# Kernel tuning notes

Hardware: AMD Instinct MI355X
Metric: run time of the kernel (lower is better)

Reference implementation:

```python
import jax, jax.numpy as jnp
import numpy as np

B, N, E = 128, 196, 2048   # batch, num_features (14x14), encoder_dim
D, A = 512, 512            # decoder_dim, attention_dim


def setup_inputs() -> dict:
    key = jax.random.key(0)
    ks = jax.random.split(key, 8)
    s_e = 1.0 / np.sqrt(E)
    s_d = 1.0 / np.sqrt(D)
    s_a = 1.0 / np.sqrt(A)
    return {
        "encoder_out": jax.random.normal(ks[0], (B, N, E), dtype=jnp.float32),
        "decoder_hidden": jax.random.normal(ks[1], (B, D), dtype=jnp.float32),
        "We": jax.random.uniform(ks[2], (E, A), jnp.float32, -s_e, s_e),
        "be": jax.random.uniform(ks[3], (A,), jnp.float32, -s_e, s_e),
        "Wd": jax.random.uniform(ks[4], (D, A), jnp.float32, -s_d, s_d),
        "bd": jax.random.uniform(ks[5], (A,), jnp.float32, -s_d, s_d),
        "Wf": jax.random.uniform(ks[6], (A, 1), jnp.float32, -s_a, s_a),
        "bf": jax.random.uniform(ks[7], (1,), jnp.float32, -s_a, s_a),
    }


def reference(encoder_out, decoder_hidden, We, be, Wd, bd, Wf, bf):
    # att1: [B,N,A] projection of encoder features
    att1 = jnp.einsum('bne,ea->bna', encoder_out, We) + be
    # att2: [B,A] projection of decoder state, broadcast over N
    att2 = decoder_hidden @ Wd + bd
    att = jnp.tanh(att1 + att2[:, None, :])          # [B,N,A]
    scores = jnp.einsum('bna,ao->bno', att, Wf) + bf  # [B,N,1]
    alpha = jax.nn.softmax(scores, axis=1)            # softmax over num_features
    context = jnp.sum(encoder_out * alpha, axis=1)    # [B,E]
    return (context, alpha)
```

## Files before the change

### kernel.cpp

```cpp
#include <hip/hip_runtime.h>
#include <hip/hip_bf16.h>
#include <stdint.h>

#define B_   128
#define N_   196
#define E_   2048
#define D_   512
#define A_   512
#define MTOT (B_ * N_)

typedef short  short8  __attribute__((ext_vector_type(8)));
typedef float  floatx4 __attribute__((ext_vector_type(4)));

__device__ __forceinline__ unsigned short f2bf(float f) {
    union { float f; uint32_t u; } v; v.f = f;
    uint32_t r = v.u + 0x7FFFu + ((v.u >> 16) & 1u);
    return (unsigned short)(r >> 16);
}

__device__ __forceinline__ uint32_t pkbf(float a, float b) {
    uint32_t ua = __float_as_uint(a) + 0x8000u;
    uint32_t ub = __float_as_uint(b) + 0x8000u;
    return __builtin_amdgcn_perm(ub, ua, 0x07060302u);
}

__global__ void transcvt_k(const float* __restrict__ We, unsigned short* __restrict__ WeT) {
    __shared__ float tile[32][33];
    const int e0 = blockIdx.x * 32, a0 = blockIdx.y * 32;
    const int t = threadIdx.x, tc = t & 31, tr = t >> 5;
#pragma unroll
    for (int i = 0; i < 4; ++i) {
        int r = tr + i * 8;
        tile[r][tc] = We[(size_t)(e0 + r) * A_ + a0 + tc];
    }
    __syncthreads();
#pragma unroll
    for (int i = 0; i < 4; ++i) {
        int r = tr + i * 8;
        WeT[(size_t)(a0 + r) * E_ + e0 + tc] = f2bf(tile[tc][r]);
    }
}

__launch_bounds__(512)
__global__ void att2_k(const float* __restrict__ dh, const float* __restrict__ Wd,
                       const float* __restrict__ bd, const float* __restrict__ be,
                       float* __restrict__ att2p) {
    const int b = blockIdx.x, t = threadIdx.x;
    __shared__ float sdh[D_];
    sdh[t] = dh[b * D_ + t];
    __syncthreads();
    float acc = 0.f;
#pragma unroll 8
    for (int d = 0; d < D_; ++d) acc += sdh[d] * Wd[(size_t)d * A_ + t];
    att2p[(size_t)b * A_ + t] = acc + bd[t] + be[t];
}

__launch_bounds__(512, 4)
__global__ void score_gemm(const float* __restrict__ enc,
                           const unsigned short* __restrict__ WeT,
                           const float* __restrict__ att2p,
                           const float* __restrict__ Wf,
                           float* __restrict__ scoresP) {
    __shared__ __align__(16) char sMem[8192 + 32768];
    __shared__ float sPart[8][64];

    const int t   = threadIdx.x;
    const int w   = t >> 6;
    const int l   = t & 63;
    const int l15 = l & 15;
    const int q4  = l >> 4;
    const int row0 = blockIdx.x * 64;

    floatx4 acc[4][4] = {};

    const float* aSrc;
    int aDst;
    {
        int s = w * 64 + l;
        int r = s >> 3, p = s & 7;
        aSrc = enc + (size_t)(row0 + r) * E_ + ((p ^ (r & 7)) * 4);
        aDst = w * 1024;
    }
    const unsigned short* bSrc[4];
    int bDst[4];
#pragma unroll
    for (int j = 0; j < 4; ++j) {
        int s = (w * 4 + j) * 64 + l;
        int n = s >> 2, p = s & 3;
        int q = p ^ ((n >> 1) & 3);
        bSrc[j] = WeT + (size_t)n * E_ + q * 8;
        bDst[j] = 8192 + (w * 4 + j) * 1024;
    }

    const int pLo   = (2 * q4) ^ (l15 & 7);
    const int offAlo = l15 * 128 + pLo * 16;
    const int offAhi = l15 * 128 + (pLo ^ 1) * 16;
    const int offB   = 8192 + (w * 64 + l15) * 64 + (q4 ^ ((l15 >> 1) & 3)) * 16;

    for (int kk = 0; kk < 64; ++kk) {
        __builtin_amdgcn_global_load_lds(
            (const __attribute__((address_space(1))) uint32_t*)(aSrc + kk * 32),
            (__attribute__((address_space(3))) uint32_t*)(sMem + aDst), 16, 0, 0);
#pragma unroll
        for (int j = 0; j < 4; ++j)
            __builtin_amdgcn_global_load_lds(
                (const __attribute__((address_space(1))) uint32_t*)(bSrc[j] + kk * 32),
                (__attribute__((address_space(3))) uint32_t*)(sMem + bDst[j]), 16, 0, 0);
        __syncthreads();

        short8 bfr[4];
        union { uint32_t u[4]; short8 s; } af[4];
#pragma unroll
        for (int ni = 0; ni < 4; ++ni)
            bfr[ni] = *(const short8*)(sMem + offB + ni * 1024);
#pragma unroll
        for (int mi = 0; mi < 4; ++mi) {
            float4 lo = *(const float4*)(sMem + offAlo + mi * 2048);
            float4 hi = *(const float4*)(sMem + offAhi + mi * 2048);
            af[mi].u[0] = pkbf(lo.x, lo.y);
            af[mi].u[1] = pkbf(lo.z, lo.w);
            af[mi].u[2] = pkbf(hi.x, hi.y);
            af[mi].u[3] = pkbf(hi.z, hi.w);
        }
#pragma unroll
        for (int mi = 0; mi < 4; ++mi) {
            acc[mi][0] = __builtin_amdgcn_mfma_f32_16x16x32_bf16(af[mi].s, bfr[0], acc[mi][0], 0, 0, 0);
            acc[mi][1] = __builtin_amdgcn_mfma_f32_16x16x32_bf16(af[mi].s, bfr[1], acc[mi][1], 0, 0, 0);
            acc[mi][2] = __builtin_amdgcn_mfma_f32_16x16x32_bf16(af[mi].s, bfr[2], acc[mi][2], 0, 0, 0);
            acc[mi][3] = __builtin_amdgcn_mfma_f32_16x16x32_bf16(af[mi].s, bfr[3], acc[mi][3], 0, 0, 0);
        }
        __syncthreads();
    }

    const int cbase = w * 64;
    float wfv[4];
#pragma unroll
    for (int ni = 0; ni < 4; ++ni) wfv[ni] = Wf[cbase + ni * 16 + l15];

#pragma unroll
    for (int mi = 0; mi < 4; ++mi) {
#pragma unroll
        for (int r = 0; r < 4; ++r) {
            const int m    = mi * 16 + q4 * 4 + r;
            const int grow = row0 + m;
            const int bb   = grow / N_;
            const float* a2 = att2p + (size_t)bb * A_ + cbase;
            float s = 0.f;
#pragma unroll
            for (int ni = 0; ni < 4; ++ni) {
                float v  = acc[mi][ni][r] + a2[ni * 16 + l15];
                float e  = __expf(2.f * v);
                float th = 1.f - 2.f / (e + 1.f);
                s += th * wfv[ni];
            }
            s += __shfl_xor(s, 1);
            s += __shfl_xor(s, 2);
            s += __shfl_xor(s, 4);
            s += __shfl_xor(s, 8);
            if (l15 == 0) sPart[w][m] = s;
        }
    }
    __syncthreads();
    if (t < 64) {
        float v = 0.f;
#pragma unroll
        for (int ww = 0; ww < 8; ++ww) v += sPart[ww][t];
        scoresP[row0 + t] = v;
    }
}

__global__ void softmax_k(const float* __restrict__ sp, float* __restrict__ alpha) {
    const int b = blockIdx.x, t = threadIdx.x;
    const int w = t >> 6, l = t & 63;
    __shared__ float red[8];
    float v = -3.0e38f;
    if (t < N_) v = sp[b * N_ + t];
    float m = v;
#pragma unroll
    for (int off = 32; off >= 1; off >>= 1) m = fmaxf(m, __shfl_xor(m, off));
    if (l == 0) red[w] = m;
    __syncthreads();
    m = fmaxf(fmaxf(red[0], red[1]), fmaxf(red[2], red[3]));
    float e = 0.f;
    if (t < N_) e = __expf(v - m);
    float s = e;
#pragma unroll
    for (int off = 32; off >= 1; off >>= 1) s += __shfl_xor(s, off);
    if (l == 0) red[4 + w] = s;
    __syncthreads();
    s = red[4] + red[5] + red[6] + red[7];
    if (t < N_) alpha[b * N_ + t] = e / s;
}

__launch_bounds__(256)
__global__ void context_k(const float* __restrict__ enc, const float* __restrict__ alpha,
                          float* __restrict__ ctx) {
    const int chunk = blockIdx.x, b = blockIdx.y;
    const int t = threadIdx.x, tn = t >> 6, tc = t & 63;
    __shared__ float  sAl[N_];
    __shared__ float4 sRed[256];
    if (t < N_) sAl[t] = alpha[b * N_ + t];
    __syncthreads();
    const float* base = enc + (size_t)b * N_ * E_ + chunk * 256 + tc * 4;
    float4 a = make_float4(0.f, 0.f, 0.f, 0.f);
#pragma unroll 7
    for (int n = tn; n < N_; n += 4) {
        float  al = sAl[n];
        float4 v  = *(const float4*)(base + (size_t)n * E_);
        a.x += al * v.x; a.y += al * v.y; a.z += al * v.z; a.w += al * v.w;
    }
    sRed[t] = a;
    __syncthreads();
    if (t < 64) {
        float4 r0 = sRed[t], r1 = sRed[t + 64], r2 = sRed[t + 128], r3 = sRed[t + 192];
        float4 o = make_float4(r0.x + r1.x + r2.x + r3.x, r0.y + r1.y + r2.y + r3.y,
                               r0.z + r1.z + r2.z + r3.z, r0.w + r1.w + r2.w + r3.w);
        *(float4*)(ctx + (size_t)b * E_ + chunk * 256 + t * 4) = o;
    }
}

extern "C" void kernel_launch(void* const* d_in, const int* in_sizes, int n_in,
                              void* d_out, int out_size, void* d_ws, size_t ws_size,
                              hipStream_t stream) {
    const float* enc = (const float*)d_in[0];
    const float* dh  = (const float*)d_in[1];
    const float* We  = (const float*)d_in[2];
    const float* be  = (const float*)d_in[3];
    const float* Wd  = (const float*)d_in[4];
    const float* bd  = (const float*)d_in[5];
    const float* Wf  = (const float*)d_in[6];

    float* out   = (float*)d_out;
    float* ctx   = out;
    float* alpha = out + B_ * E_;

    char* ws = (char*)d_ws;
    unsigned short* WeT  = (unsigned short*)ws;
    float* att2p         = (float*)(ws + (2u << 20));
    float* scoresP       = (float*)(ws + (2u << 20) + (256u << 10));

    transcvt_k <<<dim3(E_ / 32, A_ / 32), 256, 0, stream>>>(We, WeT);
    att2_k     <<<dim3(B_),              512, 0, stream>>>(dh, Wd, bd, be, att2p);
    score_gemm <<<dim3(MTOT / 64),       512, 0, stream>>>(enc, WeT, att2p, Wf, scoresP);
    softmax_k  <<<dim3(B_),              256, 0, stream>>>(scoresP, alpha);
    context_k  <<<dim3(E_ / 256, B_),    256, 0, stream>>>(enc, alpha, ctx);
}
```

Measured before the change: 440.0 us.

## Register-prefetch pipeline with bf16 double-buffered A tile and direct B loads

```diff
diff --git a/kernel.cpp b/kernel.cpp
--- a/kernel.cpp
+++ b/kernel.cpp
@@ -61,7 +61,7 @@
                            const float* __restrict__ att2p,
                            const float* __restrict__ Wf,
                            float* __restrict__ scoresP) {
-    __shared__ __align__(16) char sMem[8192 + 32768];
+    __shared__ __align__(16) unsigned short sA[2][64 * 32];
     __shared__ float sPart[8][64];
 
     const int t   = threadIdx.x;
@@ -73,66 +73,57 @@
 
     floatx4 acc[4][4] = {};
 
-    const float* aSrc;
-    int aDst;
+    const int ar = t >> 3, ac = t & 7;
+    const float* aG = enc + (size_t)(row0 + ar) * E_ + ac * 4;
+    unsigned short* aW[2] = { &sA[0][ar * 32 + ac * 4], &sA[1][ar * 32 + ac * 4] };
+    const int aRoff = l15 * 32 + q4 * 8;
+
+    const int cbase = w * 64;
+    const unsigned short* pb[4];
+#pragma unroll
+    for (int ni = 0; ni < 4; ++ni)
+        pb[ni] = WeT + (size_t)(cbase + ni * 16 + l15) * E_ + q4 * 8;
+
+    float4 Araw = *(const float4*)(aG);
+    short8 Bcur[4];
+#pragma unroll
+    for (int ni = 0; ni < 4; ++ni) Bcur[ni] = *(const short8*)(pb[ni]);
     {
-        int s = w * 64 + l;
-        int r = s >> 3, p = s & 7;
-        aSrc = enc + (size_t)(row0 + r) * E_ + ((p ^ (r & 7)) * 4);
-        aDst = w * 1024;
-    }
-    const unsigned short* bSrc[4];
-    int bDst[4];
-#pragma unroll
-    for (int j = 0; j < 4; ++j) {
-        int s = (w * 4 + j) * 64 + l;
-        int n = s >> 2, p = s & 3;
-        int q = p ^ ((n >> 1) & 3);
-        bSrc[j] = WeT + (size_t)n * E_ + q * 8;
-        bDst[j] = 8192 + (w * 4 + j) * 1024;
-    }
-
-    const int pLo   = (2 * q4) ^ (l15 & 7);
-    const int offAlo = l15 * 128 + pLo * 16;
-    const int offAhi = l15 * 128 + (pLo ^ 1) * 16;
-    const int offB   = 8192 + (w * 64 + l15) * 64 + (q4 ^ ((l15 >> 1) & 3)) * 16;
+        uint2 hv; hv.x = pkbf(Araw.x, Araw.y); hv.y = pkbf(Araw.z, Araw.w);
+        *(uint2*)aW[0] = hv;
+    }
+    Araw = *(const float4*)(aG + 32);
+    __syncthreads();
 
     for (int kk = 0; kk < 64; ++kk) {
-        __builtin_amdgcn_global_load_lds(
-            (const __attribute__((address_space(1))) uint32_t*)(aSrc + kk * 32),
-            (__attribute__((address_space(3))) uint32_t*)(sMem + aDst), 16, 0, 0);
-#pragma unroll
-        for (int j = 0; j < 4; ++j)
-            __builtin_amdgcn_global_load_lds(
-                (const __attribute__((address_space(1))) uint32_t*)(bSrc[j] + kk * 32),
-                (__attribute__((address_space(3))) uint32_t*)(sMem + bDst[j]), 16, 0, 0);
+        const unsigned short* aBuf = sA[kk & 1];
+        short8 af[4];
+#pragma unroll
+        for (int mi = 0; mi < 4; ++mi)
+            af[mi] = *(const short8*)(aBuf + aRoff + mi * 512);
+        if (kk < 63) {
+            uint2 hv; hv.x = pkbf(Araw.x, Araw.y); hv.y = pkbf(Araw.z, Araw.w);
+            *(uint2*)aW[(kk + 1) & 1] = hv;
+        }
+        if (kk < 62) Araw = *(const float4*)(aG + (kk + 2) * 32);
+        short8 Bn[4];
+        if (kk < 63) {
+#pragma unroll
+            for (int ni = 0; ni < 4; ++ni)
+                Bn[ni] = *(const short8*)(pb[ni] + (kk + 1) * 32);
+        }
+#pragma unroll
+        for (int mi = 0; mi < 4; ++mi) {
+            acc[mi][0] = __builtin_amdgcn_mfma_f32_16x16x32_bf16(af[mi], Bcur[0], acc[mi][0], 0, 0, 0);
+            acc[mi][1] = __builtin_amdgcn_mfma_f32_16x16x32_bf16(af[mi], Bcur[1], acc[mi][1], 0, 0, 0);
+            acc[mi][2] = __builtin_amdgcn_mfma_f32_16x16x32_bf16(af[mi], Bcur[2], acc[mi][2], 0, 0, 0);
+            acc[mi][3] = __builtin_amdgcn_mfma_f32_16x16x32_bf16(af[mi], Bcur[3], acc[mi][3], 0, 0, 0);
+        }
+#pragma unroll
+        for (int ni = 0; ni < 4; ++ni) Bcur[ni] = Bn[ni];
         __syncthreads();
-
-        short8 bfr[4];
-        union { uint32_t u[4]; short8 s; } af[4];
-#pragma unroll
-        for (int ni = 0; ni < 4; ++ni)
-            bfr[ni] = *(const short8*)(sMem + offB + ni * 1024);
-#pragma unroll
-        for (int mi = 0; mi < 4; ++mi) {
-            float4 lo = *(const float4*)(sMem + offAlo + mi * 2048);
-            float4 hi = *(const float4*)(sMem + offAhi + mi * 2048);
-            af[mi].u[0] = pkbf(lo.x, lo.y);
-            af[mi].u[1] = pkbf(lo.z, lo.w);
-            af[mi].u[2] = pkbf(hi.x, hi.y);
-            af[mi].u[3] = pkbf(hi.z, hi.w);
-        }
-#pragma unroll
-        for (int mi = 0; mi < 4; ++mi) {
-            acc[mi][0] = __builtin_amdgcn_mfma_f32_16x16x32_bf16(af[mi].s, bfr[0], acc[mi][0], 0, 0, 0);
-            acc[mi][1] = __builtin_amdgcn_mfma_f32_16x16x32_bf16(af[mi].s, bfr[1], acc[mi][1], 0, 0, 0);
-            acc[mi][2] = __builtin_amdgcn_mfma_f32_16x16x32_bf16(af[mi].s, bfr[2], acc[mi][2], 0, 0, 0);
-            acc[mi][3] = __builtin_amdgcn_mfma_f32_16x16x32_bf16(af[mi].s, bfr[3], acc[mi][3], 0, 0, 0);
-        }
-        __syncthreads();
-    }
-
-    const int cbase = w * 64;
+    }
+
     float wfv[4];
 #pragma unroll
     for (int ni = 0; ni < 4; ++ni) wfv[ni] = Wf[cbase + ni * 16 + l15];
```

Result: slower. 480.2 us (+9.1%).

## Split score GEMM across two column halves with pre-tiled bf16 weight layout

Applied to the files above, without the earlier changes.

```diff
diff --git a/kernel.cpp b/kernel.cpp
--- a/kernel.cpp
+++ b/kernel.cpp
@@ -24,21 +24,20 @@
     return __builtin_amdgcn_perm(ub, ua, 0x07060302u);
 }
 
-__global__ void transcvt_k(const float* __restrict__ We, unsigned short* __restrict__ WeT) {
-    __shared__ float tile[32][33];
-    const int e0 = blockIdx.x * 32, a0 = blockIdx.y * 32;
-    const int t = threadIdx.x, tc = t & 31, tr = t >> 5;
-#pragma unroll
-    for (int i = 0; i < 4; ++i) {
-        int r = tr + i * 8;
-        tile[r][tc] = We[(size_t)(e0 + r) * A_ + a0 + tc];
-    }
-    __syncthreads();
-#pragma unroll
-    for (int i = 0; i < 4; ++i) {
-        int r = tr + i * 8;
-        WeT[(size_t)(a0 + r) * E_ + e0 + tc] = f2bf(tile[tc][r]);
-    }
+__global__ void transcvt_k(const float* __restrict__ We, unsigned short* __restrict__ WeT2) {
+    const int t   = threadIdx.x;
+    const int l15 = t & 15;
+    const int q4  = (t >> 4) & 3;
+    const int g   = t >> 6;
+    const int tile = blockIdx.x;
+    const int kk   = blockIdx.y * 4 + g;
+    const int a  = tile * 16 + l15;
+    const int e0 = kk * 32 + q4 * 8;
+    union { unsigned short us[8]; short8 s; } pk;
+#pragma unroll
+    for (int j = 0; j < 8; ++j)
+        pk.us[j] = f2bf(We[(size_t)(e0 + j) * A_ + a]);
+    *(short8*)(WeT2 + (size_t)tile * 32768 + kk * 512 + q4 * 128 + l15 * 8) = pk.s;
 }
 
 __launch_bounds__(512)
@@ -55,56 +54,53 @@
     att2p[(size_t)b * A_ + t] = acc + bd[t] + be[t];
 }
 
-__launch_bounds__(512, 4)
+__launch_bounds__(256, 3)
 __global__ void score_gemm(const float* __restrict__ enc,
-                           const unsigned short* __restrict__ WeT,
+                           const unsigned short* __restrict__ WeT2,
                            const float* __restrict__ att2p,
                            const float* __restrict__ Wf,
                            float* __restrict__ scoresP) {
-    __shared__ __align__(16) char sMem[8192 + 32768];
-    __shared__ float sPart[8][64];
+    __shared__ __align__(16) char sMem[8192 + 16384];
+    __shared__ float sPart[4][64];
 
     const int t   = threadIdx.x;
     const int w   = t >> 6;
     const int l   = t & 63;
     const int l15 = l & 15;
     const int q4  = l >> 4;
-    const int row0 = blockIdx.x * 64;
+    const int row0 = blockIdx.y * 64;
+    const int col0 = blockIdx.x * 256;
 
     floatx4 acc[4][4] = {};
 
-    const float* aSrc;
-    int aDst;
-    {
-        int s = w * 64 + l;
-        int r = s >> 3, p = s & 7;
-        aSrc = enc + (size_t)(row0 + r) * E_ + ((p ^ (r & 7)) * 4);
-        aDst = w * 1024;
+    const float* aSrc[2];
+    int aDst[2];
+#pragma unroll
+    for (int h = 0; h < 2; ++h) {
+        aSrc[h] = enc + (size_t)(row0 + w * 16 + l15) * E_ + (4 * h + q4) * 4;
+        aDst[h] = w * 2048 + h * 1024 + l * 16;
     }
     const unsigned short* bSrc[4];
     int bDst[4];
 #pragma unroll
     for (int j = 0; j < 4; ++j) {
-        int s = (w * 4 + j) * 64 + l;
-        int n = s >> 2, p = s & 3;
-        int q = p ^ ((n >> 1) & 3);
-        bSrc[j] = WeT + (size_t)n * E_ + q * 8;
-        bDst[j] = 8192 + (w * 4 + j) * 1024;
-    }
-
-    const int pLo   = (2 * q4) ^ (l15 & 7);
-    const int offAlo = l15 * 128 + pLo * 16;
-    const int offAhi = l15 * 128 + (pLo ^ 1) * 16;
-    const int offB   = 8192 + (w * 64 + l15) * 64 + (q4 ^ ((l15 >> 1) & 3)) * 16;
+        bSrc[j] = WeT2 + (size_t)((col0 >> 4) + w * 4 + j) * 32768 + l * 8;
+        bDst[j] = 8192 + (w * 4 + j) * 1024 + l * 16;
+    }
+
+    const int offAlo = (2 * q4) * 256 + l15 * 16;
+    const int offB   = 8192 + w * 4096 + q4 * 256 + l15 * 16;
 
     for (int kk = 0; kk < 64; ++kk) {
-        __builtin_amdgcn_global_load_lds(
-            (const __attribute__((address_space(1))) uint32_t*)(aSrc + kk * 32),
-            (__attribute__((address_space(3))) uint32_t*)(sMem + aDst), 16, 0, 0);
+#pragma unroll
+        for (int h = 0; h < 2; ++h)
+            __builtin_amdgcn_global_load_lds(
+                (const __attribute__((address_space(1))) uint32_t*)(aSrc[h] + kk * 32),
+                (__attribute__((address_space(3))) uint32_t*)(sMem + aDst[h]), 16, 0, 0);
 #pragma unroll
         for (int j = 0; j < 4; ++j)
             __builtin_amdgcn_global_load_lds(
-                (const __attribute__((address_space(1))) uint32_t*)(bSrc[j] + kk * 32),
+                (const __attribute__((address_space(1))) uint32_t*)(bSrc[j] + kk * 512),
                 (__attribute__((address_space(3))) uint32_t*)(sMem + bDst[j]), 16, 0, 0);
         __syncthreads();
 
@@ -115,8 +111,8 @@
             bfr[ni] = *(const short8*)(sMem + offB + ni * 1024);
 #pragma unroll
         for (int mi = 0; mi < 4; ++mi) {
-            float4 lo = *(const float4*)(sMem + offAlo + mi * 2048);
-            float4 hi = *(const float4*)(sMem + offAhi + mi * 2048);
+            float4 lo = *(const float4*)(sMem + mi * 2048 + offAlo);
+            float4 hi = *(const float4*)(sMem + mi * 2048 + offAlo + 256);
             af[mi].u[0] = pkbf(lo.x, lo.y);
             af[mi].u[1] = pkbf(lo.z, lo.w);
             af[mi].u[2] = pkbf(hi.x, hi.y);
@@ -132,7 +128,7 @@
         __syncthreads();
     }
 
-    const int cbase = w * 64;
+    const int cbase = col0 + w * 64;
     float wfv[4];
 #pragma unroll
     for (int ni = 0; ni < 4; ++ni) wfv[ni] = Wf[cbase + ni * 16 + l15];
@@ -162,10 +158,8 @@
     }
     __syncthreads();
     if (t < 64) {
-        float v = 0.f;
-#pragma unroll
-        for (int ww = 0; ww < 8; ++ww) v += sPart[ww][t];
-        scoresP[row0 + t] = v;
+        float v = sPart[0][t] + sPart[1][t] + sPart[2][t] + sPart[3][t];
+        scoresP[(size_t)blockIdx.x * MTOT + row0 + t] = v;
     }
 }
 
@@ -174,7 +168,7 @@
     const int w = t >> 6, l = t & 63;
     __shared__ float red[8];
     float v = -3.0e38f;
-    if (t < N_) v = sp[b * N_ + t];
+    if (t < N_) v = sp[b * N_ + t] + sp[MTOT + b * N_ + t];
     float m = v;
 #pragma unroll
     for (int off = 32; off >= 1; off >>= 1) m = fmaxf(m, __shfl_xor(m, off));
@@ -235,13 +229,13 @@
     float* alpha = out + B_ * E_;
 
     char* ws = (char*)d_ws;
-    unsigned short* WeT  = (unsigned short*)ws;
+    unsigned short* WeT2 = (unsigned short*)ws;
     float* att2p         = (float*)(ws + (2u << 20));
     float* scoresP       = (float*)(ws + (2u << 20) + (256u << 10));
 
-    transcvt_k <<<dim3(E_ / 32, A_ / 32), 256, 0, stream>>>(We, WeT);
-    att2_k     <<<dim3(B_),              512, 0, stream>>>(dh, Wd, bd, be, att2p);
-    score_gemm <<<dim3(MTOT / 64),       512, 0, stream>>>(enc, WeT, att2p, Wf, scoresP);
-    softmax_k  <<<dim3(B_),              256, 0, stream>>>(scoresP, alpha);
-    context_k  <<<dim3(E_ / 256, B_),    256, 0, stream>>>(enc, alpha, ctx);
-}
+    transcvt_k <<<dim3(32, 16),       256, 0, stream>>>(We, WeT2);
+    att2_k     <<<dim3(B_),           512, 0, stream>>>(dh, Wd, bd, be, att2p);
+    score_gemm <<<dim3(2, MTOT / 64), 256, 0, stream>>>(enc, WeT2, att2p, Wf, scoresP);
+    softmax_k  <<<dim3(B_),           256, 0, stream>>>(scoresP, alpha);
+    context_k  <<<dim3(E_ / 256, B_), 256, 0, stream>>>(enc, alpha, ctx);
+}
```

Result: slower. 466.2 us (+6.0%).
